# Performance work log

Measured on AMD Instinct MI355X. Metric: run time of the kernel, lower is better.

Reference implementation:

```python
import jax, jax.numpy as jnp
import numpy as np

B, T, E, L, D = 8, 512, 1024, 8, 512
EPS = 1e-5


def _ln(x, g, b):
    m = x.mean(-1, keepdims=True)
    v = ((x - m) ** 2).mean(-1, keepdims=True)
    return (x - m) * jax.lax.rsqrt(v + EPS) * g + b


def setup_inputs() -> dict:
    key = jax.random.key(0)
    ks = jax.random.split(key, 16)
    s = lambda k, shape, scale: (jax.random.normal(k, shape, dtype=jnp.float32) * scale)
    inp = {
        "embedded_input": jax.random.normal(ks[0], (B, T, E), dtype=jnp.float32),
        # [L, D, D] recurrence parameter tensors (xavier-ish init)
        "state_control": s(ks[1], (L, D, D), (2.0 / (2 * D)) ** 0.5),
        "input_influence": s(ks[2], (L, D, D), (2.0 / (2 * D)) ** 0.5),
        "output_shaper": s(ks[3], (L, D, D), (2.0 / (2 * D)) ** 0.5),
        # per-layer GLU projections D -> 2D, stacked; weights stored (in, out)
        "glu_w": s(ks[4], (L, D, 2 * D), (1.0 / D) ** 0.5),
        "glu_b": jnp.zeros((L, 2 * D), jnp.float32),
        # embedding_to_state: E -> L*D
        "e2s_w": s(ks[5], (E, L * D), (1.0 / E) ** 0.5),
        "e2s_b": jnp.zeros((L * D,), jnp.float32),
        # shared layernorms
        "ln_glu_g": jnp.ones((D,), jnp.float32), "ln_glu_b": jnp.zeros((D,), jnp.float32),
        "ln_state_g": jnp.ones((D,), jnp.float32), "ln_state_b": jnp.zeros((D,), jnp.float32),
        "ln_emb_g": jnp.ones((E,), jnp.float32), "ln_emb_b": jnp.zeros((E,), jnp.float32),
        # per-layer feed-forward: LN(D) -> Linear(D,D) -> GELU -> Linear(D,E)
        "ff_ln_g": jnp.ones((L, D), jnp.float32), "ff_ln_b": jnp.zeros((L, D), jnp.float32),
        "ff_w1": s(ks[6], (L, D, D), (1.0 / D) ** 0.5), "ff_b1": jnp.zeros((L, D), jnp.float32),
        "ff_w2": s(ks[7], (L, D, E), (1.0 / D) ** 0.5), "ff_b2": jnp.zeros((L, E), jnp.float32),
        # layer attention scorer E -> 1
        "attn_w": s(ks[8], (E, 1), (1.0 / E) ** 0.5), "attn_b": jnp.zeros((1,), jnp.float32),
    }
    return inp


def reference(embedded_input, state_control, input_influence, output_shaper,
              glu_w, glu_b, e2s_w, e2s_b,
              ln_glu_g, ln_glu_b, ln_state_g, ln_state_b, ln_emb_g, ln_emb_b,
              ff_ln_g, ff_ln_b, ff_w1, ff_b1, ff_w2, ff_b2, attn_w, attn_b):
    # einsum('bld,lds->bld') keeps d in output and sums s => elementwise scale by row-sums
    sc_sum = state_control.sum(-1)    # [L, D]
    ii_sum = input_influence.sum(-1)  # [L, D]
    os_sum = output_shaper.sum(-1)    # [L, D]

    # embedding_to_state -> [B, T, L, D], scan over time
    tokens = (embedded_input @ e2s_w + e2s_b).reshape(B, T, L, D)
    tokens = tokens.transpose(1, 0, 2, 3)  # [T, B, L, D]

    def step(last, tok):
        h = last * sc_sum + tok * ii_sum                    # [B, L, D]
        hn = _ln(h, ln_glu_g, ln_glu_b)
        proj = jnp.einsum('bld,lde->ble', hn, glu_w) + glu_b  # [B, L, 2D]
        a, g = jnp.split(proj, 2, axis=-1)
        new = _ln(a * jax.nn.sigmoid(g), ln_state_g, ln_state_b)
        return new, new

    last0 = jnp.zeros((B, L, D), embedded_input.dtype)
    _, states = jax.lax.scan(step, last0, tokens)           # [T, B, L, D]
    states = states.transpose(1, 0, 2, 3)                   # [B, T, L, D]

    attn_out = states * os_sum                              # [B, T, L, D]

    # per-layer feed-forward (exact GELU, as torch default)
    y = _ln(attn_out, ff_ln_g, ff_ln_b)
    h = jax.nn.gelu(jnp.einsum('btld,lde->btle', y, ff_w1) + ff_b1, approximate=False)
    layer_outputs = jnp.einsum('btld,lde->btle', h, ff_w2) + ff_b2  # [B, T, L, E]

    scores = jax.nn.softmax((layer_outputs @ attn_w)[..., 0] + attn_b[0], axis=2)  # over layers
    weighted = (layer_outputs * scores[..., None]).sum(axis=2)      # [B, T, E]
    return _ln(weighted, ln_emb_g, ln_emb_b)
```

## Files before the change

kernel.cpp:

```cpp
#include <hip/hip_runtime.h>
#include <hip/hip_bf16.h>
#include <math.h>

static constexpr int nB = 8, nT = 512, nE = 1024, nL = 8, nD = 512;
static constexpr int nBT = nB * nT;
static constexpr int nLD = nL * nD;

typedef __attribute__((ext_vector_type(8))) short short8v;
typedef __attribute__((ext_vector_type(4))) float f32x4;
typedef __attribute__((ext_vector_type(4))) unsigned int u32x4;

__device__ __forceinline__ unsigned short f2bf(float f) {
    unsigned int u = __float_as_uint(f);
    return (unsigned short)((u + 0x7fffu + ((u >> 16) & 1u)) >> 16);
}
__device__ __forceinline__ float bfu2f(unsigned short u) {
    return __uint_as_float(((unsigned int)u) << 16);
}
__device__ __forceinline__ float gelu_f(float x) {
    return 0.5f * x * (1.0f + erff(x * 0.70710678118654752f));
}

__global__ __launch_bounds__(256) void k_wdot(const float* __restrict__ src,
                                              const float* __restrict__ w,
                                              float* __restrict__ dst,
                                              int rows, int rowlen) {
    int row = blockIdx.x * 4 + (threadIdx.x >> 6);
    if (row >= rows) return;
    int lane = threadIdx.x & 63;
    const float* p = src + (size_t)row * rowlen;
    float s = 0.f;
    if (w) { for (int i = lane; i < rowlen; i += 64) s += p[i] * w[i]; }
    else   { for (int i = lane; i < rowlen; i += 64) s += p[i]; }
#pragma unroll
    for (int off = 32; off > 0; off >>= 1) s += __shfl_down(s, off, 64);
    if (lane == 0) dst[row] = s;
}

__global__ __launch_bounds__(256) void k_init2(unsigned int* recs) {
    int i = blockIdx.x * 256 + threadIdx.x;
    if (i < 2 * nL * nB * 128)
        __hip_atomic_store(recs + i * 4 + 3, 0u,
                           __ATOMIC_RELAXED, __HIP_MEMORY_SCOPE_AGENT);
}

__global__ __launch_bounds__(256) void k_cast(const float* __restrict__ s,
                                              unsigned short* __restrict__ d, int n) {
    int idx = (blockIdx.x * 256 + threadIdx.x) * 4;
    if (idx >= n) return;
    float4 v = *reinterpret_cast<const float4*>(s + idx);
    ushort4 o;
    o.x = f2bf(v.x); o.y = f2bf(v.y); o.z = f2bf(v.z); o.w = f2bf(v.w);
    *reinterpret_cast<ushort4*>(d + idx) = o;
}

__global__ __launch_bounds__(256) void k_transp(const float* __restrict__ src,
                                                unsigned short* __restrict__ dst,
                                                int R, int Cc,
                                                long long sSrc, long long sDst) {
    src += (size_t)blockIdx.z * sSrc;
    dst += (size_t)blockIdx.z * sDst;
    __shared__ float t[32][33];
    const int tx = threadIdx.x & 31, ty = threadIdx.x >> 5;
    const int r0 = blockIdx.y * 32, c0 = blockIdx.x * 32;
#pragma unroll
    for (int r = 0; r < 4; ++r)
        t[ty + r * 8][tx] = src[(size_t)(r0 + ty + r * 8) * Cc + c0 + tx];
    __syncthreads();
#pragma unroll
    for (int r = 0; r < 4; ++r)
        dst[(size_t)(c0 + ty + r * 8) * R + r0 + tx] = f2bf(t[tx][ty + r * 8]);
}

__global__ __launch_bounds__(256) void k_pack2(const float* __restrict__ src,
                                               uint4* __restrict__ dst) {
    const int blk = blockIdx.x;
    const int w = blk & 7, q = (blk >> 3) & 7, l = blk >> 6;
    const float* wl = src + (size_t)l * nD * 1024;
    for (int i = threadIdx.x; i < 16 * 64; i += 256) {
        const int kt = i >> 6, ln = i & 63;
        const int j = ln & 15, g = ln >> 4;
        const int u = j >> 1;
        const int col = (j & 1) ? (512 + q * 64 + w * 8 + u)
                                : (q * 64 + w * 8 + u);
        const int k0 = 32 * kt + 8 * g;
        unsigned pr[4];
#pragma unroll
        for (int p = 0; p < 4; ++p) {
            float a = wl[(size_t)(k0 + 2 * p) * 1024 + col];
            float c = wl[(size_t)(k0 + 2 * p + 1) * 1024 + col];
            pr[p] = (unsigned)f2bf(a) | ((unsigned)f2bf(c) << 16);
        }
        dst[((((size_t)l * 8 + q) * 8 + w) * 16 + kt) * 64 + ln] =
            make_uint4(pr[0], pr[1], pr[2], pr[3]);
    }
}

template<int ACT>
__global__ __launch_bounds__(256) void k_gemm_bf(
    const unsigned short* __restrict__ A, int lda, long long sA,
    const unsigned short* __restrict__ Bt, int ldb, long long sB,
    const float* __restrict__ bias, long long sBias,
    float* __restrict__ C, int ldc, long long sC,
    int M, int N, int K)
{
    A  += (size_t)blockIdx.z * sA;
    Bt += (size_t)blockIdx.z * sB;
    C  += (size_t)blockIdx.z * sC;
    const float* biasp = bias ? bias + (size_t)blockIdx.z * sBias : nullptr;

    __shared__ __align__(16) unsigned short A_s[128][40];
    __shared__ __align__(16) unsigned short B_s[128][40];
    const int tid = threadIdx.x, lane = tid & 63;
    const int wv = tid >> 6;
    const int wm = (wv >> 1) * 64, wn = (wv & 1) * 64;
    const int bm = blockIdx.y * 128, bn = blockIdx.x * 128;
    const int srow = tid >> 2, sc8 = (tid & 3) * 8;

    f32x4 acc[4][4];
#pragma unroll
    for (int i = 0; i < 4; ++i)
#pragma unroll
        for (int j = 0; j < 4; ++j) acc[i][j] = f32x4{0.f, 0.f, 0.f, 0.f};

    const int fr = lane & 15, fg = (lane >> 4) * 8;

    for (int kt = 0; kt < K; kt += 32) {
        uint4 a0 = *reinterpret_cast<const uint4*>(A + (size_t)(bm + srow) * lda + kt + sc8);
        uint4 a1 = *reinterpret_cast<const uint4*>(A + (size_t)(bm + srow + 64) * lda + kt + sc8);
        uint4 b0 = *reinterpret_cast<const uint4*>(Bt + (size_t)(bn + srow) * ldb + kt + sc8);
        uint4 b1 = *reinterpret_cast<const uint4*>(Bt + (size_t)(bn + srow + 64) * ldb + kt + sc8);
        __syncthreads();
        *reinterpret_cast<uint4*>(&A_s[srow][sc8]) = a0;
        *reinterpret_cast<uint4*>(&A_s[srow + 64][sc8]) = a1;
        *reinterpret_cast<uint4*>(&B_s[srow][sc8]) = b0;
        *reinterpret_cast<uint4*>(&B_s[srow + 64][sc8]) = b1;
        __syncthreads();
        short8v af[4], bf[4];
#pragma unroll
        for (int mi = 0; mi < 4; ++mi)
            af[mi] = *reinterpret_cast<const short8v*>(&A_s[wm + mi * 16 + fr][fg]);
#pragma unroll
        for (int ni = 0; ni < 4; ++ni)
            bf[ni] = *reinterpret_cast<const short8v*>(&B_s[wn + ni * 16 + fr][fg]);
#pragma unroll
        for (int mi = 0; mi < 4; ++mi)
#pragma unroll
            for (int ni = 0; ni < 4; ++ni)
                acc[mi][ni] = __builtin_amdgcn_mfma_f32_16x16x32_bf16(
                    af[mi], bf[ni], acc[mi][ni], 0, 0, 0);
    }

#pragma unroll
    for (int mi = 0; mi < 4; ++mi)
#pragma unroll
        for (int ni = 0; ni < 4; ++ni) {
            const int col = bn + wn + ni * 16 + (lane & 15);
            const float bv = biasp ? biasp[col] : 0.f;
#pragma unroll
            for (int p = 0; p < 4; ++p) {
                const int row = bm + wm + mi * 16 + (lane >> 4) * 4 + p;
                float v = acc[mi][ni][p] + bv;
                if (ACT == 1) v = gelu_f(v);
                C[(size_t)row * ldc + col] = v;
            }
        }
}

__global__ __launch_bounds__(512, 1) void k_scan7(
    const float* __restrict__ tokens,
    const uint4* __restrict__ wswz,
    const float* __restrict__ glu_b,
    const float* __restrict__ sc_sum, const float* __restrict__ ii_sum,
    const float* __restrict__ ln_glu_g, const float* __restrict__ ln_glu_b,
    const float* __restrict__ ln_state_g, const float* __restrict__ ln_state_b,
    float* __restrict__ vout,
    unsigned int* __restrict__ recs)
{
    const int l = blockIdx.x & 7, q = blockIdx.x >> 3;
    const int tid = threadIdx.x, w = tid >> 6, lane = tid & 63;
    const int b = w;

    __shared__ __align__(16) unsigned hn_pk[8][260];
    __shared__ __align__(16) unsigned zbuf[4];
    __shared__ __align__(16) unsigned short vrow[8][512];
    __shared__ __align__(16) unsigned short vstage[8][64];
    __shared__ __align__(16) float vsq[8][8][2];

    uint4 wr[16];
    {
        const uint4* wp = wswz + ((((size_t)l * 8 + q) * 8 + w) * 16) * 64 + lane;
#pragma unroll
        for (int kt = 0; kt < 16; ++kt) wr[kt] = wp[kt * 64];
    }
    const int d0 = lane * 8;
    float P_sc[8], P_ii[8], P_gg[8], P_gb[8], P_sg[8], P_sb[8];
#pragma unroll
    for (int j = 0; j < 8; j += 4) {
        *reinterpret_cast<float4*>(&P_sc[j]) = *reinterpret_cast<const float4*>(sc_sum + l * nD + d0 + j);
        *reinterpret_cast<float4*>(&P_ii[j]) = *reinterpret_cast<const float4*>(ii_sum + l * nD + d0 + j);
        *reinterpret_cast<float4*>(&P_gg[j]) = *reinterpret_cast<const float4*>(ln_glu_g + d0 + j);
        *reinterpret_cast<float4*>(&P_gb[j]) = *reinterpret_cast<const float4*>(ln_glu_b + d0 + j);
        *reinterpret_cast<float4*>(&P_sg[j]) = *reinterpret_cast<const float4*>(ln_state_g + d0 + j);
        *reinterpret_cast<float4*>(&P_sb[j]) = *reinterpret_cast<const float4*>(ln_state_b + d0 + j);
    }
    const int cu = (lane & 15) >> 1;
    const int mycol = (lane & 1) ? (512 + q * 64 + w * 8 + cu)
                                 : (q * 64 + w * 8 + cu);
    const float bias_c = glu_b[l * 1024 + mycol];
    const int vcol = q * 64 + w * 8 + cu;

    if (tid < 4) zbuf[tid] = 0u;

    const float* tokp = tokens + ((size_t)b * nT * nL + l) * nD + d0;

    const unsigned* afp; int astep;
    {
        int bb = lane & 15, g = lane >> 4;
        if (bb < 8) { afp = &hn_pk[bb][g * 4]; astep = 16; }
        else        { afp = &zbuf[0];          astep = 0;  }
    }
    __syncthreads();

    float4 tk0 = *reinterpret_cast<const float4*>(tokp);
    float4 tk1 = *reinterpret_cast<const float4*>(tokp + 4);

    for (int t = 0; t < nT; ++t) {
        float tk[8] = {tk0.x, tk0.y, tk0.z, tk0.w, tk1.x, tk1.y, tk1.z, tk1.w};
        float h[8];
        if (t > 0) {
            const unsigned* rp = recs + ((((size_t)((t - 1) & 1) * nL + l) * nB + b) * 128) * 4;
            const unsigned* pa = rp + lane * 4;
            const unsigned* pb = rp + (lane + 64) * 4;
            u32x4 ra, rb;
            int ok;
            do {
                asm volatile(
                    "global_load_dwordx4 %0, %2, off sc0 sc1\n\t"
                    "global_load_dwordx4 %1, %3, off sc0 sc1\n\t"
                    "s_waitcnt vmcnt(0)"
                    : "=&v"(ra), "=&v"(rb)
                    : "v"(pa), "v"(pb)
                    : "memory");
                ok = (ra[3] == (unsigned)t) && (rb[3] == (unsigned)t);
            } while (!__all(ok));

            float S = 0.f, Q = 0.f;
            if (lane & 1) {
                S = __uint_as_float(ra[1]) + __uint_as_float(rb[1]);
                Q = __uint_as_float(ra[2]) + __uint_as_float(rb[2]);
            }
#pragma unroll
            for (int o = 32; o > 0; o >>= 1) { S += __shfl_xor(S, o, 64); Q += __shfl_xor(Q, o, 64); }
            const float mv = S * (1.f / nD);
            const float iv = rsqrtf(Q * (1.f / nD) - mv * mv + 1e-5f);

            {
                const int ia = lane, ib2 = lane + 64;
                const int qa = ia >> 4, wa = (ia >> 1) & 7, ja = ia & 1;
                const int qb2 = ib2 >> 4, wb2 = (ib2 >> 1) & 7;
                unsigned* da = reinterpret_cast<unsigned*>(&vrow[b][qa * 64 + wa * 8 + ja * 6]);
                unsigned* db = reinterpret_cast<unsigned*>(&vrow[b][qb2 * 64 + wb2 * 8 + ja * 6]);
                if (!ja) {
                    da[0] = ra[0]; da[1] = ra[1]; da[2] = ra[2];
                    db[0] = rb[0]; db[1] = rb[1]; db[2] = rb[2];
                } else {
                    da[0] = ra[0];
                    db[0] = rb[0];
                }
            }
            asm volatile("s_waitcnt lgkmcnt(0)" ::: "memory");
            __builtin_amdgcn_sched_barrier(0);
            uint4 pv = *reinterpret_cast<const uint4*>(&vrow[b][lane * 8]);
            float vv[8];
            vv[0] = bfu2f((unsigned short)(pv.x & 0xffffu));
            vv[1] = bfu2f((unsigned short)(pv.x >> 16));
            vv[2] = bfu2f((unsigned short)(pv.y & 0xffffu));
            vv[3] = bfu2f((unsigned short)(pv.y >> 16));
            vv[4] = bfu2f((unsigned short)(pv.z & 0xffffu));
            vv[5] = bfu2f((unsigned short)(pv.z >> 16));
            vv[6] = bfu2f((unsigned short)(pv.w & 0xffffu));
            vv[7] = bfu2f((unsigned short)(pv.w >> 16));
#pragma unroll
            for (int j = 0; j < 8; ++j) {
                float st = (vv[j] - mv) * iv * P_sg[j] + P_sb[j];
                h[j] = st * P_sc[j] + tk[j] * P_ii[j];
            }
        } else {
#pragma unroll
            for (int j = 0; j < 8; ++j) h[j] = tk[j] * P_ii[j];
        }

        if (t + 1 < nT) {
            tk0 = *reinterpret_cast<const float4*>(tokp + (size_t)(t + 1) * nLD);
            tk1 = *reinterpret_cast<const float4*>(tokp + (size_t)(t + 1) * nLD + 4);
        }

        float S = 0.f, Q = 0.f;
#pragma unroll
        for (int j = 0; j < 8; ++j) { S += h[j]; Q += h[j] * h[j]; }
#pragma unroll
        for (int o = 32; o > 0; o >>= 1) { S += __shfl_xor(S, o, 64); Q += __shfl_xor(Q, o, 64); }
        const float mh = S * (1.f / nD);
        const float ih = rsqrtf(Q * (1.f / nD) - mh * mh + 1e-5f);
        unsigned pr[4];
#pragma unroll
        for (int p = 0; p < 4; ++p) {
            float a0 = (h[2 * p]     - mh) * ih * P_gg[2 * p]     + P_gb[2 * p];
            float a1 = (h[2 * p + 1] - mh) * ih * P_gg[2 * p + 1] + P_gb[2 * p + 1];
            pr[p] = (unsigned)f2bf(a0) | ((unsigned)f2bf(a1) << 16);
        }
        *reinterpret_cast<uint4*>(&hn_pk[b][lane * 4]) = make_uint4(pr[0], pr[1], pr[2], pr[3]);

        asm volatile("s_waitcnt lgkmcnt(0)" ::: "memory");
        __builtin_amdgcn_s_barrier();
        __builtin_amdgcn_sched_barrier(0);

        f32x4 acc0 = {0.f, 0.f, 0.f, 0.f}, acc1 = {0.f, 0.f, 0.f, 0.f};
#pragma unroll
        for (int kt = 0; kt < 8; ++kt) {
            short8v a0 = *reinterpret_cast<const short8v*>(afp + (2 * kt) * astep);
            short8v a1 = *reinterpret_cast<const short8v*>(afp + (2 * kt + 1) * astep);
            acc0 = __builtin_amdgcn_mfma_f32_16x16x32_bf16(
                a0, __builtin_bit_cast(short8v, wr[2 * kt]), acc0, 0, 0, 0);
            acc1 = __builtin_amdgcn_mfma_f32_16x16x32_bf16(
                a1, __builtin_bit_cast(short8v, wr[2 * kt + 1]), acc1, 0, 0, 0);
        }

        float x[4], y[4];
#pragma unroll
        for (int i = 0; i < 4; ++i) x[i] = acc0[i] + acc1[i] + bias_c;
#pragma unroll
        for (int i = 0; i < 4; ++i) y[i] = __shfl_xor(x[i], 1, 64);
        float sv[4], sq[4];
        const int r0 = (lane >> 4) * 4;
        const bool prod = (lane < 32) && !(lane & 1);
#pragma unroll
        for (int i = 0; i < 4; ++i) {
            float v = x[i] / (1.f + __expf(-y[i]));
            sv[i] = prod ? v : 0.f;
            sq[i] = prod ? v * v : 0.f;
            if (prod) {
                vout[(((size_t)(r0 + i) * nT + t) * nL + l) * nD + vcol] = v;
                vstage[r0 + i][w * 8 + cu] = f2bf(v);
            }
        }
#pragma unroll
        for (int i = 0; i < 4; ++i) {
            sv[i] += __shfl_xor(sv[i], 2, 64); sq[i] += __shfl_xor(sq[i], 2, 64);
            sv[i] += __shfl_xor(sv[i], 4, 64); sq[i] += __shfl_xor(sq[i], 4, 64);
            sv[i] += __shfl_xor(sv[i], 8, 64); sq[i] += __shfl_xor(sq[i], 8, 64);
        }
        if (lane == 0 || lane == 16) {
#pragma unroll
            for (int i = 0; i < 4; ++i) {
                vsq[r0 + i][w][0] = sv[i];
                vsq[r0 + i][w][1] = sq[i];
            }
        }

        asm volatile("s_waitcnt lgkmcnt(0)" ::: "memory");
        __builtin_amdgcn_s_barrier();
        __builtin_amdgcn_sched_barrier(0);

        if (tid < 128) {
            const int bb = tid >> 4, wb = (tid >> 1) & 7, jb = tid & 1;
            const unsigned* vp = reinterpret_cast<const unsigned*>(&vstage[bb][wb * 8]);
            u32x4 rec;
            if (!jb) { rec[0] = vp[0]; rec[1] = vp[1]; rec[2] = vp[2]; }
            else {
                rec[0] = vp[3];
                rec[1] = __float_as_uint(vsq[bb][wb][0]);
                rec[2] = __float_as_uint(vsq[bb][wb][1]);
            }
            rec[3] = (unsigned)(t + 1);
            unsigned* dst = recs + (((((size_t)(t & 1) * nL + l) * nB + bb) * 128)
                                    + q * 16 + wb * 2 + jb) * 4;
            asm volatile("global_store_dwordx4 %0, %1, off sc0 sc1"
                         :: "v"(dst), "v"(rec) : "memory");
        }
    }
}

__global__ __launch_bounds__(256) void k_y2(
    const float* __restrict__ vout, const float* __restrict__ os_sum,
    const float* __restrict__ lsg, const float* __restrict__ lsb,
    const float* __restrict__ fg, const float* __restrict__ fb,
    unsigned short* __restrict__ y)
{
    const int row = blockIdx.x * 4 + (threadIdx.x >> 6);
    const int lane = threadIdx.x & 63;
    const int l = row & 7;

    const float* vp = vout + (size_t)row * nD;
    const int base = lane * 8;
    float vv[8];
    *reinterpret_cast<float4*>(&vv[0]) = *reinterpret_cast<const float4*>(vp + base);
    *reinterpret_cast<float4*>(&vv[4]) = *reinterpret_cast<const float4*>(vp + base + 4);
    float S = 0.f, Q = 0.f;
#pragma unroll
    for (int j = 0; j < 8; ++j) { S += vv[j]; Q += vv[j] * vv[j]; }
#pragma unroll
    for (int o = 32; o > 0; o >>= 1) { S += __shfl_xor(S, o, 64); Q += __shfl_xor(Q, o, 64); }
    const float mv = S * (1.f / nD);
    const float iv = rsqrtf(Q * (1.f / nD) - mv * mv + 1e-5f);

    const float* op = os_sum + l * nD;
    float val[8];
    float s2 = 0.f, q2 = 0.f;
#pragma unroll
    for (int j = 0; j < 8; j += 4) {
        float4 o4 = *reinterpret_cast<const float4*>(op + base + j);
        float4 g4 = *reinterpret_cast<const float4*>(lsg + base + j);
        float4 b4 = *reinterpret_cast<const float4*>(lsb + base + j);
        val[j]     = ((vv[j]     - mv) * iv * g4.x + b4.x) * o4.x;
        val[j + 1] = ((vv[j + 1] - mv) * iv * g4.y + b4.y) * o4.y;
        val[j + 2] = ((vv[j + 2] - mv) * iv * g4.z + b4.z) * o4.z;
        val[j + 3] = ((vv[j + 3] - mv) * iv * g4.w + b4.w) * o4.w;
    }
#pragma unroll
    for (int j = 0; j < 8; ++j) { s2 += val[j]; q2 += val[j] * val[j]; }
#pragma unroll
    for (int o = 32; o > 0; o >>= 1) { s2 += __shfl_xor(s2, o, 64); q2 += __shfl_xor(q2, o, 64); }
    const float m2 = s2 * (1.f / nD);
    const float i2 = rsqrtf(q2 * (1.f / nD) - m2 * m2 + 1e-5f);
    const float* gp = fg + l * nD;
    const float* bp = fb + l * nD;
    unsigned short* yp = y + (size_t)row * nD;
    unsigned pk[4];
#pragma unroll
    for (int j = 0; j < 8; j += 4) {
        float4 g4 = *reinterpret_cast<const float4*>(gp + base + j);
        float4 b4 = *reinterpret_cast<const float4*>(bp + base + j);
        float o0 = (val[j]     - m2) * i2 * g4.x + b4.x;
        float o1 = (val[j + 1] - m2) * i2 * g4.y + b4.y;
        float o2 = (val[j + 2] - m2) * i2 * g4.z + b4.z;
        float o3 = (val[j + 3] - m2) * i2 * g4.w + b4.w;
        pk[j / 4 * 2]     = (unsigned)f2bf(o0) | ((unsigned)f2bf(o1) << 16);
        pk[j / 4 * 2 + 1] = (unsigned)f2bf(o2) | ((unsigned)f2bf(o3) << 16);
    }
    *reinterpret_cast<uint4*>(yp + base) = make_uint4(pk[0], pk[1], pk[2], pk[3]);
}

__global__ __launch_bounds__(256) void k_scores(
    const float* __restrict__ h, const float* __restrict__ w2a,
    const float* __restrict__ c2, const float* __restrict__ attn_b,
    unsigned short* __restrict__ hbf, float* __restrict__ scores)
{
    const int bt = blockIdx.x;
    const int tid = threadIdx.x, wid = tid >> 6, lane = tid & 63;
    __shared__ float slog[nL];
    const float* hrow = h + (size_t)bt * nLD;
    for (int l = wid; l < nL; l += 4) {
        const float* hp = hrow + l * nD;
        const float* wp = w2a + l * nD;
        float s = 0.f;
        for (int i = lane; i < nD; i += 64) s += hp[i] * wp[i];
#pragma unroll
        for (int off = 32; off > 0; off >>= 1) s += __shfl_down(s, off, 64);
        if (lane == 0) slog[l] = s + c2[l] + attn_b[0];
    }
    __syncthreads();
    float mx = -1e30f;
#pragma unroll
    for (int l = 0; l < nL; ++l) mx = fmaxf(mx, slog[l]);
    float den = 0.f;
#pragma unroll
    for (int l = 0; l < nL; ++l) den += __expf(slog[l] - mx);
    float rden = 1.f / den;
    unsigned short* obase = hbf + (size_t)bt * nLD;
#pragma unroll
    for (int it = 0; it < 4; ++it) {
        int idx = tid * 4 + it * 1024;
        int l = idx >> 9;
        float s = __expf(slog[l] - mx) * rden;
        float4 v = *reinterpret_cast<const float4*>(hrow + idx);
        unsigned p0 = (unsigned)f2bf(v.x * s) | ((unsigned)f2bf(v.y * s) << 16);
        unsigned p1 = (unsigned)f2bf(v.z * s) | ((unsigned)f2bf(v.w * s) << 16);
        *reinterpret_cast<uint2*>(obase + idx) = make_uint2(p0, p1);
    }
    if (tid < nL) scores[bt * nL + tid] = __expf(slog[tid] - mx) * rden;
}

__global__ __launch_bounds__(256) void k_final(
    const float* __restrict__ wbuf, const float* __restrict__ scores,
    const float* __restrict__ ff_b2, const float* __restrict__ g,
    const float* __restrict__ bvec, float* __restrict__ out)
{
    const int bt = blockIdx.x;
    const int tid = threadIdx.x;
    __shared__ float ssc[nL];
    __shared__ float red[8];
    if (tid < nL) ssc[tid] = scores[bt * nL + tid];
    __syncthreads();
    const int e0 = tid * 4;
    float4 w = *reinterpret_cast<const float4*>(wbuf + (size_t)bt * nE + e0);
#pragma unroll
    for (int l = 0; l < nL; ++l) {
        float s = ssc[l];
        float4 b2 = *reinterpret_cast<const float4*>(ff_b2 + l * nE + e0);
        w.x += s * b2.x; w.y += s * b2.y; w.z += s * b2.z; w.w += s * b2.w;
    }
    float sum = w.x + w.y + w.z + w.w;
    float sq = w.x * w.x + w.y * w.y + w.z * w.z + w.w * w.w;
    int wid = tid >> 6, lane = tid & 63;
#pragma unroll
    for (int off = 32; off > 0; off >>= 1) {
        sum += __shfl_down(sum, off, 64); sq += __shfl_down(sq, off, 64);
    }
    if (lane == 0) { red[wid] = sum; red[4 + wid] = sq; }
    __syncthreads();
    sum = red[0] + red[1] + red[2] + red[3];
    sq  = red[4] + red[5] + red[6] + red[7];
    float mean = sum * (1.f / nE);
    float inv = rsqrtf(sq * (1.f / nE) - mean * mean + 1e-5f);
    float4 g4 = *reinterpret_cast<const float4*>(g + e0);
    float4 b4 = *reinterpret_cast<const float4*>(bvec + e0);
    float4 o;
    o.x = (w.x - mean) * inv * g4.x + b4.x;
    o.y = (w.y - mean) * inv * g4.y + b4.y;
    o.z = (w.z - mean) * inv * g4.z + b4.z;
    o.w = (w.w - mean) * inv * g4.w + b4.w;
    *reinterpret_cast<float4*>(out + (size_t)bt * nE + e0) = o;
}

extern "C" void kernel_launch(void* const* d_in, const int* in_sizes, int n_in,
                              void* d_out, int out_size, void* d_ws, size_t ws_size,
                              hipStream_t stream) {
    (void)in_sizes; (void)n_in; (void)out_size; (void)ws_size;
    const float* emb            = (const float*)d_in[0];
    const float* state_control  = (const float*)d_in[1];
    const float* input_influence= (const float*)d_in[2];
    const float* output_shaper  = (const float*)d_in[3];
    const float* glu_w          = (const float*)d_in[4];
    const float* glu_b          = (const float*)d_in[5];
    const float* e2s_w          = (const float*)d_in[6];
    const float* e2s_b          = (const float*)d_in[7];
    const float* ln_glu_g       = (const float*)d_in[8];
    const float* ln_glu_b       = (const float*)d_in[9];
    const float* ln_state_g     = (const float*)d_in[10];
    const float* ln_state_b     = (const float*)d_in[11];
    const float* ln_emb_g       = (const float*)d_in[12];
    const float* ln_emb_b       = (const float*)d_in[13];
    const float* ff_ln_g        = (const float*)d_in[14];
    const float* ff_ln_b        = (const float*)d_in[15];
    const float* ff_w1          = (const float*)d_in[16];
    const float* ff_b1          = (const float*)d_in[17];
    const float* ff_w2          = (const float*)d_in[18];
    const float* ff_b2          = (const float*)d_in[19];
    const float* attn_w         = (const float*)d_in[20];
    const float* attn_b         = (const float*)d_in[21];

    char* ws = (char*)d_ws;
    float* tokens = (float*)ws;  ws += (size_t)nBT * nLD * 4;
    float* vbuf   = (float*)ws;  ws += (size_t)nBT * nLD * 4;
    uint4* wswz   = (uint4*)ws;  ws += (size_t)nL * 8 * 8 * 16 * 64 * 16;
    unsigned int* recs = (unsigned int*)ws; ws += (size_t)2 * nL * nB * 128 * 16;
    unsigned short* w1T = (unsigned short*)ws; ws += (size_t)nL * nD * nD * 2;
    unsigned short* w2T = (unsigned short*)ws; ws += (size_t)nE * nLD * 2;
    float* sc_sum = (float*)ws;  ws += nLD * 4;
    float* ii_sum = (float*)ws;  ws += nLD * 4;
    float* os_sum = (float*)ws;  ws += nLD * 4;
    float* w2a    = (float*)ws;  ws += nLD * 4;
    float* c2     = (float*)ws;  ws += 256;
    float* scores = (float*)ws;  ws += (size_t)nBT * nL * 4;
    unsigned short* emb_bf = (unsigned short*)vbuf;
    unsigned short* e2sT   = (unsigned short*)vbuf + (size_t)nBT * nE;
    unsigned short* ybf    = (unsigned short*)tokens;
    unsigned short* hbf    = (unsigned short*)tokens + (size_t)nBT * nLD;
    float* wbuf = tokens;

    k_init2<<<64, 256, 0, stream>>>(recs);
    k_pack2<<<nL * 64, 256, 0, stream>>>(glu_w, wswz);
    k_wdot<<<1024, 256, 0, stream>>>(state_control, nullptr, sc_sum, nLD, nD);
    k_wdot<<<1024, 256, 0, stream>>>(input_influence, nullptr, ii_sum, nLD, nD);
    k_wdot<<<1024, 256, 0, stream>>>(output_shaper, nullptr, os_sum, nLD, nD);
    k_wdot<<<1024, 256, 0, stream>>>(ff_w2, attn_w, w2a, nLD, nE);
    k_wdot<<<2, 256, 0, stream>>>(ff_b2, attn_w, c2, nL, nE);
    k_cast<<<nBT * nE / 1024, 256, 0, stream>>>(emb, emb_bf, nBT * nE);
    k_transp<<<dim3(nLD / 32, nE / 32, 1), 256, 0, stream>>>(e2s_w, e2sT, nE, nLD, 0, 0);
    k_transp<<<dim3(nD / 32, nD / 32, nL), 256, 0, stream>>>(ff_w1, w1T, nD, nD,
                                                             (long long)nD * nD, (long long)nD * nD);
    k_transp<<<dim3(nE / 32, nLD / 32, 1), 256, 0, stream>>>(ff_w2, w2T, nLD, nE, 0, 0);

    k_gemm_bf<0><<<dim3(32, 32, 1), 256, 0, stream>>>(
        emb_bf, nE, 0, e2sT, nE, 0, e2s_b, 0, tokens, nLD, 0, nBT, nLD, nE);

    k_scan7<<<64, 512, 0, stream>>>(tokens, wswz, glu_b, sc_sum, ii_sum,
                                    ln_glu_g, ln_glu_b, ln_state_g, ln_state_b,
                                    vbuf, recs);

    k_y2<<<nBT * nL / 4, 256, 0, stream>>>(vbuf, os_sum,
                                           ln_state_g, ln_state_b,
                                           ff_ln_g, ff_ln_b, ybf);

    k_gemm_bf<1><<<dim3(4, 32, 8), 256, 0, stream>>>(
        ybf, nLD, nD, w1T, nD, (long long)nD * nD, ff_b1, nD,
        vbuf, nLD, nD, nBT, nD, nD);

    k_scores<<<nBT, 256, 0, stream>>>(vbuf, w2a, c2, attn_b, hbf, scores);

    k_gemm_bf<0><<<dim3(8, 32, 1), 256, 0, stream>>>(
        hbf, nLD, 0, w2T, nLD, 0, nullptr, 0, wbuf, nE, 0, nBT, nE, nLD);

    k_final<<<nBT, 256, 0, stream>>>(wbuf, scores, ff_b2, ln_emb_g, ln_emb_b, (float*)d_out);
}
```

Measured before the change: 2.172 ms.

## Fuse state LayerNorm and FF LayerNorm into the scan, dropping the fp32 state output

The scan kernel now produces the bf16 FF-input activations directly. At each step it takes the previous step's gathered state, applies the state LN, scales by os_sum, applies the per-layer FF LN and stores a bf16 row. A tail block handles the last timestep. This removes the per-step fp32 state stores and the separate k_y2 kernel with its round trip through a large buffer. In exchange, each serial scan step does extra reductions, and the FF LN now sees bf16-rounded states instead of fp32 ones. Workspace aliasing is rearranged so ybf and hbf share vbuf and the GELU output lives in tokens.

```diff
diff --git a/kernel.cpp b/kernel.cpp
--- a/kernel.cpp
+++ b/kernel.cpp
@@ -167,14 +167,16 @@
         }
 }
 
-__global__ __launch_bounds__(512, 1) void k_scan7(
+__global__ __launch_bounds__(512, 1) void k_scan8(
     const float* __restrict__ tokens,
     const uint4* __restrict__ wswz,
     const float* __restrict__ glu_b,
     const float* __restrict__ sc_sum, const float* __restrict__ ii_sum,
+    const float* __restrict__ os_sum,
     const float* __restrict__ ln_glu_g, const float* __restrict__ ln_glu_b,
     const float* __restrict__ ln_state_g, const float* __restrict__ ln_state_b,
-    float* __restrict__ vout,
+    const float* __restrict__ ff_ln_g, const float* __restrict__ ff_ln_b,
+    unsigned short* __restrict__ ybf,
     unsigned int* __restrict__ recs)
 {
     const int l = blockIdx.x & 7, q = blockIdx.x >> 3;
@@ -195,20 +197,23 @@
     }
     const int d0 = lane * 8;
     float P_sc[8], P_ii[8], P_gg[8], P_gb[8], P_sg[8], P_sb[8];
+    float P_os[8], P_fg[8], P_fb[8];
 #pragma unroll
     for (int j = 0; j < 8; j += 4) {
         *reinterpret_cast<float4*>(&P_sc[j]) = *reinterpret_cast<const float4*>(sc_sum + l * nD + d0 + j);
         *reinterpret_cast<float4*>(&P_ii[j]) = *reinterpret_cast<const float4*>(ii_sum + l * nD + d0 + j);
+        *reinterpret_cast<float4*>(&P_os[j]) = *reinterpret_cast<const float4*>(os_sum + l * nD + d0 + j);
         *reinterpret_cast<float4*>(&P_gg[j]) = *reinterpret_cast<const float4*>(ln_glu_g + d0 + j);
         *reinterpret_cast<float4*>(&P_gb[j]) = *reinterpret_cast<const float4*>(ln_glu_b + d0 + j);
         *reinterpret_cast<float4*>(&P_sg[j]) = *reinterpret_cast<const float4*>(ln_state_g + d0 + j);
         *reinterpret_cast<float4*>(&P_sb[j]) = *reinterpret_cast<const float4*>(ln_state_b + d0 + j);
+        *reinterpret_cast<float4*>(&P_fg[j]) = *reinterpret_cast<const float4*>(ff_ln_g + l * nD + d0 + j);
+        *reinterpret_cast<float4*>(&P_fb[j]) = *reinterpret_cast<const float4*>(ff_ln_b + l * nD + d0 + j);
     }
     const int cu = (lane & 15) >> 1;
     const int mycol = (lane & 1) ? (512 + q * 64 + w * 8 + cu)
                                  : (q * 64 + w * 8 + cu);
     const float bias_c = glu_b[l * 1024 + mycol];
-    const int vcol = q * 64 + w * 8 + cu;
 
     if (tid < 4) zbuf[tid] = 0u;
 
@@ -224,6 +229,8 @@
 
     float4 tk0 = *reinterpret_cast<const float4*>(tokp);
     float4 tk1 = *reinterpret_cast<const float4*>(tokp + 4);
+
+    float vvC[8], mvC = 0.f, ivC = 0.f;
 
     for (int t = 0; t < nT; ++t) {
         float tk[8] = {tk0.x, tk0.y, tk0.z, tk0.w, tk1.x, tk1.y, tk1.z, tk1.w};
@@ -252,8 +259,8 @@
             }
 #pragma unroll
             for (int o = 32; o > 0; o >>= 1) { S += __shfl_xor(S, o, 64); Q += __shfl_xor(Q, o, 64); }
-            const float mv = S * (1.f / nD);
-            const float iv = rsqrtf(Q * (1.f / nD) - mv * mv + 1e-5f);
+            mvC = S * (1.f / nD);
+            ivC = rsqrtf(Q * (1.f / nD) - mvC * mvC + 1e-5f);
 
             {
                 const int ia = lane, ib2 = lane + 64;
@@ -272,18 +279,17 @@
             asm volatile("s_waitcnt lgkmcnt(0)" ::: "memory");
             __builtin_amdgcn_sched_barrier(0);
             uint4 pv = *reinterpret_cast<const uint4*>(&vrow[b][lane * 8]);
-            float vv[8];
-            vv[0] = bfu2f((unsigned short)(pv.x & 0xffffu));
-            vv[1] = bfu2f((unsigned short)(pv.x >> 16));
-            vv[2] = bfu2f((unsigned short)(pv.y & 0xffffu));
-            vv[3] = bfu2f((unsigned short)(pv.y >> 16));
-            vv[4] = bfu2f((unsigned short)(pv.z & 0xffffu));
-            vv[5] = bfu2f((unsigned short)(pv.z >> 16));
-            vv[6] = bfu2f((unsigned short)(pv.w & 0xffffu));
-            vv[7] = bfu2f((unsigned short)(pv.w >> 16));
+            vvC[0] = bfu2f((unsigned short)(pv.x & 0xffffu));
+            vvC[1] = bfu2f((unsigned short)(pv.x >> 16));
+            vvC[2] = bfu2f((unsigned short)(pv.y & 0xffffu));
+            vvC[3] = bfu2f((unsigned short)(pv.y >> 16));
+            vvC[4] = bfu2f((unsigned short)(pv.z & 0xffffu));
+            vvC[5] = bfu2f((unsigned short)(pv.z >> 16));
+            vvC[6] = bfu2f((unsigned short)(pv.w & 0xffffu));
+            vvC[7] = bfu2f((unsigned short)(pv.w >> 16));
 #pragma unroll
             for (int j = 0; j < 8; ++j) {
-                float st = (vv[j] - mv) * iv * P_sg[j] + P_sb[j];
+                float st = (vvC[j] - mvC) * ivC * P_sg[j] + P_sb[j];
                 h[j] = st * P_sc[j] + tk[j] * P_ii[j];
             }
         } else {
@@ -340,10 +346,7 @@
             float v = x[i] / (1.f + __expf(-y[i]));
             sv[i] = prod ? v : 0.f;
             sq[i] = prod ? v * v : 0.f;
-            if (prod) {
-                vout[(((size_t)(r0 + i) * nT + t) * nL + l) * nD + vcol] = v;
-                vstage[r0 + i][w * 8 + cu] = f2bf(v);
-            }
+            if (prod) vstage[r0 + i][w * 8 + cu] = f2bf(v);
         }
 #pragma unroll
         for (int i = 0; i < 4; ++i) {
@@ -379,67 +382,105 @@
             asm volatile("global_store_dwordx4 %0, %1, off sc0 sc1"
                          :: "v"(dst), "v"(rec) : "memory");
         }
-    }
-}
-
-__global__ __launch_bounds__(256) void k_y2(
-    const float* __restrict__ vout, const float* __restrict__ os_sum,
-    const float* __restrict__ lsg, const float* __restrict__ lsb,
-    const float* __restrict__ fg, const float* __restrict__ fb,
-    unsigned short* __restrict__ y)
-{
-    const int row = blockIdx.x * 4 + (threadIdx.x >> 6);
-    const int lane = threadIdx.x & 63;
-    const int l = row & 7;
-
-    const float* vp = vout + (size_t)row * nD;
-    const int base = lane * 8;
-    float vv[8];
-    *reinterpret_cast<float4*>(&vv[0]) = *reinterpret_cast<const float4*>(vp + base);
-    *reinterpret_cast<float4*>(&vv[4]) = *reinterpret_cast<const float4*>(vp + base + 4);
-    float S = 0.f, Q = 0.f;
-#pragma unroll
-    for (int j = 0; j < 8; ++j) { S += vv[j]; Q += vv[j] * vv[j]; }
-#pragma unroll
-    for (int o = 32; o > 0; o >>= 1) { S += __shfl_xor(S, o, 64); Q += __shfl_xor(Q, o, 64); }
-    const float mv = S * (1.f / nD);
-    const float iv = rsqrtf(Q * (1.f / nD) - mv * mv + 1e-5f);
-
-    const float* op = os_sum + l * nD;
-    float val[8];
-    float s2 = 0.f, q2 = 0.f;
-#pragma unroll
-    for (int j = 0; j < 8; j += 4) {
-        float4 o4 = *reinterpret_cast<const float4*>(op + base + j);
-        float4 g4 = *reinterpret_cast<const float4*>(lsg + base + j);
-        float4 b4 = *reinterpret_cast<const float4*>(lsb + base + j);
-        val[j]     = ((vv[j]     - mv) * iv * g4.x + b4.x) * o4.x;
-        val[j + 1] = ((vv[j + 1] - mv) * iv * g4.y + b4.y) * o4.y;
-        val[j + 2] = ((vv[j + 2] - mv) * iv * g4.z + b4.z) * o4.z;
-        val[j + 3] = ((vv[j + 3] - mv) * iv * g4.w + b4.w) * o4.w;
-    }
-#pragma unroll
-    for (int j = 0; j < 8; ++j) { s2 += val[j]; q2 += val[j] * val[j]; }
-#pragma unroll
-    for (int o = 32; o > 0; o >>= 1) { s2 += __shfl_xor(s2, o, 64); q2 += __shfl_xor(q2, o, 64); }
-    const float m2 = s2 * (1.f / nD);
-    const float i2 = rsqrtf(q2 * (1.f / nD) - m2 * m2 + 1e-5f);
-    const float* gp = fg + l * nD;
-    const float* bp = fb + l * nD;
-    unsigned short* yp = y + (size_t)row * nD;
-    unsigned pk[4];
-#pragma unroll
-    for (int j = 0; j < 8; j += 4) {
-        float4 g4 = *reinterpret_cast<const float4*>(gp + base + j);
-        float4 b4 = *reinterpret_cast<const float4*>(bp + base + j);
-        float o0 = (val[j]     - m2) * i2 * g4.x + b4.x;
-        float o1 = (val[j + 1] - m2) * i2 * g4.y + b4.y;
-        float o2 = (val[j + 2] - m2) * i2 * g4.z + b4.z;
-        float o3 = (val[j + 3] - m2) * i2 * g4.w + b4.w;
-        pk[j / 4 * 2]     = (unsigned)f2bf(o0) | ((unsigned)f2bf(o1) << 16);
-        pk[j / 4 * 2 + 1] = (unsigned)f2bf(o2) | ((unsigned)f2bf(o3) << 16);
-    }
-    *reinterpret_cast<uint4*>(yp + base) = make_uint4(pk[0], pk[1], pk[2], pk[3]);
+
+        if (t > 0) {
+            float val[8], S2 = 0.f, Q2 = 0.f;
+#pragma unroll
+            for (int j = 0; j < 8; ++j) {
+                float st = (vvC[j] - mvC) * ivC * P_sg[j] + P_sb[j];
+                val[j] = st * P_os[j];
+                S2 += val[j]; Q2 += val[j] * val[j];
+            }
+#pragma unroll
+            for (int o = 32; o > 0; o >>= 1) { S2 += __shfl_xor(S2, o, 64); Q2 += __shfl_xor(Q2, o, 64); }
+            const float m2 = S2 * (1.f / nD);
+            const float i2 = rsqrtf(Q2 * (1.f / nD) - m2 * m2 + 1e-5f);
+            unsigned pk[4];
+#pragma unroll
+            for (int p = 0; p < 4; ++p) {
+                float o0 = (val[2 * p]     - m2) * i2 * P_fg[2 * p]     + P_fb[2 * p];
+                float o1 = (val[2 * p + 1] - m2) * i2 * P_fg[2 * p + 1] + P_fb[2 * p + 1];
+                pk[p] = (unsigned)f2bf(o0) | ((unsigned)f2bf(o1) << 16);
+            }
+            *reinterpret_cast<uint4*>(ybf + (((size_t)b * nT + (t - 1)) * nL + l) * nD + d0) =
+                make_uint4(pk[0], pk[1], pk[2], pk[3]);
+        }
+    }
+
+    {
+        const unsigned tagf = (unsigned)nT;
+        const unsigned* rp = recs + ((((size_t)((nT - 1) & 1) * nL + l) * nB + b) * 128) * 4;
+        const unsigned* pa = rp + lane * 4;
+        const unsigned* pb = rp + (lane + 64) * 4;
+        u32x4 ra, rb;
+        int ok;
+        do {
+            asm volatile(
+                "global_load_dwordx4 %0, %2, off sc0 sc1\n\t"
+                "global_load_dwordx4 %1, %3, off sc0 sc1\n\t"
+                "s_waitcnt vmcnt(0)"
+                : "=&v"(ra), "=&v"(rb)
+                : "v"(pa), "v"(pb)
+                : "memory");
+            ok = (ra[3] == tagf) && (rb[3] == tagf);
+        } while (!__all(ok));
+
+        float S = 0.f, Q = 0.f;
+        if (lane & 1) {
+            S = __uint_as_float(ra[1]) + __uint_as_float(rb[1]);
+            Q = __uint_as_float(ra[2]) + __uint_as_float(rb[2]);
+        }
+#pragma unroll
+        for (int o = 32; o > 0; o >>= 1) { S += __shfl_xor(S, o, 64); Q += __shfl_xor(Q, o, 64); }
+        const float mv = S * (1.f / nD);
+        const float iv = rsqrtf(Q * (1.f / nD) - mv * mv + 1e-5f);
+        {
+            const int ia = lane, ib2 = lane + 64;
+            const int qa = ia >> 4, wa = (ia >> 1) & 7, ja = ia & 1;
+            const int qb2 = ib2 >> 4, wb2 = (ib2 >> 1) & 7;
+            unsigned* da = reinterpret_cast<unsigned*>(&vrow[b][qa * 64 + wa * 8 + ja * 6]);
+            unsigned* db = reinterpret_cast<unsigned*>(&vrow[b][qb2 * 64 + wb2 * 8 + ja * 6]);
+            if (!ja) {
+                da[0] = ra[0]; da[1] = ra[1]; da[2] = ra[2];
+                db[0] = rb[0]; db[1] = rb[1]; db[2] = rb[2];
+            } else {
+                da[0] = ra[0];
+                db[0] = rb[0];
+            }
+        }
+        asm volatile("s_waitcnt lgkmcnt(0)" ::: "memory");
+        __builtin_amdgcn_sched_barrier(0);
+        uint4 pv = *reinterpret_cast<const uint4*>(&vrow[b][lane * 8]);
+        float vv[8];
+        vv[0] = bfu2f((unsigned short)(pv.x & 0xffffu));
+        vv[1] = bfu2f((unsigned short)(pv.x >> 16));
+        vv[2] = bfu2f((unsigned short)(pv.y & 0xffffu));
+        vv[3] = bfu2f((unsigned short)(pv.y >> 16));
+        vv[4] = bfu2f((unsigned short)(pv.z & 0xffffu));
+        vv[5] = bfu2f((unsigned short)(pv.z >> 16));
+        vv[6] = bfu2f((unsigned short)(pv.w & 0xffffu));
+        vv[7] = bfu2f((unsigned short)(pv.w >> 16));
+        float val[8], S2 = 0.f, Q2 = 0.f;
+#pragma unroll
+        for (int j = 0; j < 8; ++j) {
+            float st = (vv[j] - mv) * iv * P_sg[j] + P_sb[j];
+            val[j] = st * P_os[j];
+            S2 += val[j]; Q2 += val[j] * val[j];
+        }
+#pragma unroll
+        for (int o = 32; o > 0; o >>= 1) { S2 += __shfl_xor(S2, o, 64); Q2 += __shfl_xor(Q2, o, 64); }
+        const float m2 = S2 * (1.f / nD);
+        const float i2 = rsqrtf(Q2 * (1.f / nD) - m2 * m2 + 1e-5f);
+        unsigned pk[4];
+#pragma unroll
+        for (int p = 0; p < 4; ++p) {
+            float o0 = (val[2 * p]     - m2) * i2 * P_fg[2 * p]     + P_fb[2 * p];
+            float o1 = (val[2 * p + 1] - m2) * i2 * P_fg[2 * p + 1] + P_fb[2 * p + 1];
+            pk[p] = (unsigned)f2bf(o0) | ((unsigned)f2bf(o1) << 16);
+        }
+        *reinterpret_cast<uint4*>(ybf + (((size_t)b * nT + (nT - 1)) * nL + l) * nD + d0) =
+            make_uint4(pk[0], pk[1], pk[2], pk[3]);
+    }
 }
 
 __global__ __launch_bounds__(256) void k_scores(
@@ -566,9 +607,10 @@
     float* scores = (float*)ws;  ws += (size_t)nBT * nL * 4;
     unsigned short* emb_bf = (unsigned short*)vbuf;
     unsigned short* e2sT   = (unsigned short*)vbuf + (size_t)nBT * nE;
-    unsigned short* ybf    = (unsigned short*)tokens;
-    unsigned short* hbf    = (unsigned short*)tokens + (size_t)nBT * nLD;
-    float* wbuf = tokens;
+    unsigned short* ybf    = (unsigned short*)vbuf;
+    float* hfull           = tokens;
+    unsigned short* hbf    = (unsigned short*)vbuf;
+    float* wbuf            = tokens;
 
     k_init2<<<64, 256, 0, stream>>>(recs);
     k_pack2<<<nL * 64, 256, 0, stream>>>(glu_w, wswz);
@@ -586,19 +628,15 @@
     k_gemm_bf<0><<<dim3(32, 32, 1), 256, 0, stream>>>(
         emb_bf, nE, 0, e2sT, nE, 0, e2s_b, 0, tokens, nLD, 0, nBT, nLD, nE);
 
-    k_scan7<<<64, 512, 0, stream>>>(tokens, wswz, glu_b, sc_sum, ii_sum,
+    k_scan8<<<64, 512, 0, stream>>>(tokens, wswz, glu_b, sc_sum, ii_sum, os_sum,
                                     ln_glu_g, ln_glu_b, ln_state_g, ln_state_b,
-                                    vbuf, recs);
-
-    k_y2<<<nBT * nL / 4, 256, 0, stream>>>(vbuf, os_sum,
-                                           ln_state_g, ln_state_b,
-                                           ff_ln_g, ff_ln_b, ybf);
+                                    ff_ln_g, ff_ln_b, ybf, recs);
 
     k_gemm_bf<1><<<dim3(4, 32, 8), 256, 0, stream>>>(
         ybf, nLD, nD, w1T, nD, (long long)nD * nD, ff_b1, nD,
-        vbuf, nLD, nD, nBT, nD, nD);
-
-    k_scores<<<nBT, 256, 0, stream>>>(vbuf, w2a, c2, attn_b, hbf, scores);
+        hfull, nLD, nD, nBT, nD, nD);
+
+    k_scores<<<nBT, 256, 0, stream>>>(hfull, w2a, c2, attn_b, hbf, scores);
 
     k_gemm_bf<0><<<dim3(8, 32, 1), 256, 0, stream>>>(
         hbf, nLD, 0, w2T, nLD, 0, nullptr, 0, wbuf, nE, 0, nBT, nE, nLD);
```

Result: faster. 2.004 ms (-7.8%).
